# Performance work log

Measured on AMD Instinct MI355X. Metric: run time of the kernel, lower is better.

Reference implementation:

```python
import jax, jax.numpy as jnp
import numpy as np

NUM_GRAPHS = 64
BN_EPS = 1e-5
N, E, F_IN, ED, HID, HEADS, NC = 50000, 1600000, 128, 16, 32, 2, 2


def gatv2(x, src, dst, edge_attr, Wl, bl, Wr, br, We, att, bias, num_nodes):
    """PyG GATv2Conv: gather, leaky-relu score, segment softmax over dst, scatter-sum."""
    H, C = att.shape
    xl = (x @ Wl + bl).reshape(num_nodes, H, C)  # source transform (lin_l)
    xr = (x @ Wr + br).reshape(num_nodes, H, C)  # target transform (lin_r)
    ef = (edge_attr @ We).reshape(-1, H, C)      # [E,H,C]
    m = xl[src] + xr[dst] + ef                   # per-edge message pre-activation
    m = jnp.where(m > 0, m, 0.2 * m)             # LeakyReLU(0.2)
    score = jnp.einsum('ehc,hc->eh', m, att)     # [E,H]
    smax = jax.ops.segment_max(score, dst, num_segments=num_nodes)
    smax = jnp.where(jnp.isfinite(smax), smax, 0.0)
    ex = jnp.exp(score - smax[dst])
    denom = jax.ops.segment_sum(ex, dst, num_segments=num_nodes)
    alpha = ex / (denom[dst] + 1e-16)            # segment softmax
    out = jax.ops.segment_sum(xl[src] * alpha[..., None], dst, num_segments=num_nodes)
    return out.reshape(num_nodes, H * C) + bias


def batchnorm(x, gamma, beta, mean, var):
    # inference-mode BatchNorm1d with running statistics
    return (x - mean) * gamma * jax.lax.rsqrt(var + BN_EPS) + beta


def setup_inputs() -> dict:
    keys = jax.random.split(jax.random.key(0), 40)
    ki = iter(keys)

    def glorot(shape):
        return jax.random.normal(next(ki), shape, jnp.float32) / np.sqrt(shape[0])

    def bn_params(dim):
        g = jax.random.uniform(next(ki), (dim,), jnp.float32, 0.5, 1.5)
        b = jax.random.normal(next(ki), (dim,), jnp.float32) * 0.1
        m = jax.random.normal(next(ki), (dim,), jnp.float32) * 0.1
        v = jax.random.uniform(next(ki), (dim,), jnp.float32, 0.5, 1.5)
        return g, b, m, v

    x = jax.random.normal(next(ki), (N, F_IN), jnp.float32)
    edge_index = jax.random.randint(next(ki), (2, E), 0, N)
    edge_attr = jax.random.normal(next(ki), (E, ED), jnp.float32)
    batch = jnp.sort(jax.random.randint(next(ki), (N,), 0, NUM_GRAPHS))

    d1 = HID * HEADS  # 64
    inp = dict(x=x, edge_attr=edge_attr, edge_index=edge_index, batch=batch)
    # conv1: in=F_IN, heads=HEADS, out=HID
    inp.update(c1_Wl=glorot((F_IN, d1)), c1_bl=jnp.zeros((d1,), jnp.float32),
               c1_Wr=glorot((F_IN, d1)), c1_br=jnp.zeros((d1,), jnp.float32),
               c1_We=glorot((ED, d1)),
               c1_att=jax.random.normal(next(ki), (HEADS, HID), jnp.float32) / np.sqrt(HID),
               c1_bias=jnp.zeros((d1,), jnp.float32))
    g, b, m, v = bn_params(d1)
    inp.update(bn1_gamma=g, bn1_beta=b, bn1_mean=m, bn1_var=v)
    inp.update(sp1_W=glorot((F_IN, d1)), sp1_b=jnp.zeros((d1,), jnp.float32))
    # conv2: in=d1, heads=1, out=HID
    inp.update(c2_Wl=glorot((d1, HID)), c2_bl=jnp.zeros((HID,), jnp.float32),
               c2_Wr=glorot((d1, HID)), c2_br=jnp.zeros((HID,), jnp.float32),
               c2_We=glorot((ED, HID)),
               c2_att=jax.random.normal(next(ki), (1, HID), jnp.float32) / np.sqrt(HID),
               c2_bias=jnp.zeros((HID,), jnp.float32))
    g, b, m, v = bn_params(HID)
    inp.update(bn2_gamma=g, bn2_beta=b, bn2_mean=m, bn2_var=v)
    inp.update(sp2_W=glorot((d1, HID)), sp2_b=jnp.zeros((HID,), jnp.float32))
    inp.update(cls_W=glorot((2 * HID, NC)), cls_b=jnp.zeros((NC,), jnp.float32))
    return inp


def reference(x, edge_attr,
              c1_Wl, c1_bl, c1_Wr, c1_br, c1_We, c1_att, c1_bias,
              bn1_gamma, bn1_beta, bn1_mean, bn1_var, sp1_W, sp1_b,
              c2_Wl, c2_bl, c2_Wr, c2_br, c2_We, c2_att, c2_bias,
              bn2_gamma, bn2_beta, bn2_mean, bn2_var, sp2_W, sp2_b,
              cls_W, cls_b, edge_index, batch):
    num_nodes = x.shape[0]
    src, dst = edge_index[0], edge_index[1]

    xp = x @ sp1_W + sp1_b
    h = gatv2(x, src, dst, edge_attr, c1_Wl, c1_bl, c1_Wr, c1_br, c1_We, c1_att, c1_bias, num_nodes)
    h = batchnorm(h, bn1_gamma, bn1_beta, bn1_mean, bn1_var)
    h = jax.nn.elu(h + xp)

    xp = h @ sp2_W + sp2_b
    h2 = gatv2(h, src, dst, edge_attr, c2_Wl, c2_bl, c2_Wr, c2_br, c2_We, c2_att, c2_bias, num_nodes)
    h2 = batchnorm(h2, bn2_gamma, bn2_beta, bn2_mean, bn2_var)
    h2 = jax.nn.elu(h2 + xp)

    # global mean + max pool per graph
    cnt = jax.ops.segment_sum(jnp.ones((num_nodes, 1), h2.dtype), batch, num_segments=NUM_GRAPHS)
    gmean = jax.ops.segment_sum(h2, batch, num_segments=NUM_GRAPHS) / jnp.maximum(cnt, 1.0)
    gmax = jax.ops.segment_max(h2, batch, num_segments=NUM_GRAPHS)
    gmax = jnp.where(jnp.isfinite(gmax), gmax, 0.0)
    g = jnp.concatenate([gmean, gmax], axis=1)
    # dropout is identity in eval mode
    return g @ cls_W + cls_b
```

## Files before the change

### kernel.cpp

```cpp
#include <hip/hip_runtime.h>
#include <math.h>

#define NN 50000
#define NE 1600000
#define FIN 128
#define EDIM 16
#define DD1 64
#define HH1 2
#define DD2 32
#define NG 64
#define NCLS 2
#define SCAN_CHUNK 512
#define NB_SCAN ((NN + SCAN_CHUNK - 1) / SCAN_CHUNK)

template<int IN, int OUT>
__global__ __launch_bounds__(256) void transform_k(const float* __restrict__ X,
    const float* __restrict__ W, const float* __restrict__ b,
    float* __restrict__ out, int n) {
  constexpr int NPB = 32;
  constexpr int TPN = 256 / NPB;
  constexpr int CPT = OUT / TPN;
  __shared__ float sW[IN * OUT];
  __shared__ float sX[NPB * IN];
  int t = threadIdx.x;
  int nodeBase = blockIdx.x * NPB;
  for (int i = t; i < IN * OUT; i += 256) sW[i] = W[i];
  constexpr int XE = NPB * IN / 4;
  const float4* X4 = (const float4*)X;
  float4* sX4 = (float4*)sX;
  for (int i = t; i < XE; i += 256) {
    int node = nodeBase + i / (IN / 4);
    sX4[i] = (node < n) ? X4[(size_t)node * (IN / 4) + i % (IN / 4)]
                        : make_float4(0.f, 0.f, 0.f, 0.f);
  }
  __syncthreads();
  int ln = t / TPN;
  int cb = (t % TPN) * CPT;
  int node = nodeBase + ln;
  float acc[CPT];
#pragma unroll
  for (int j = 0; j < CPT; j++) acc[j] = b[cb + j];
  const float* xs = &sX[ln * IN];
  for (int k = 0; k < IN; k++) {
    float xv = xs[k];
#pragma unroll
    for (int j = 0; j < CPT; j++) acc[j] += xv * sW[k * OUT + cb + j];
  }
  if (node < n) {
#pragma unroll
    for (int j = 0; j < CPT; j++) out[(size_t)node * OUT + cb + j] = acc[j];
  }
}

__global__ __launch_bounds__(256) void hist_k(const int* __restrict__ ei, int* __restrict__ deg) {
  int e = blockIdx.x * 256 + threadIdx.x;
  if (e >= NE) return;
  atomicAdd(&deg[ei[NE + e]], 1);
}

__global__ __launch_bounds__(256) void scan_bsum_k(const int* __restrict__ deg,
                                                   int* __restrict__ bsum, int n) {
  __shared__ int s[256];
  int b = blockIdx.x, t = threadIdx.x;
  int i0 = b * SCAN_CHUNK + 2 * t, i1 = i0 + 1;
  int v = ((i0 < n) ? deg[i0] : 0) + ((i1 < n) ? deg[i1] : 0);
  s[t] = v;
  __syncthreads();
  for (int off = 128; off; off >>= 1) {
    if (t < off) s[t] += s[t + off];
    __syncthreads();
  }
  if (t == 0) bsum[b] = s[0];
}

__global__ void scan_boff_k(const int* __restrict__ bsum, int* __restrict__ boff, int nb) {
  if (threadIdx.x == 0) {
    int run = 0;
    for (int i = 0; i < nb; i++) { int v = bsum[i]; boff[i] = run; run += v; }
  }
}

__global__ __launch_bounds__(256) void scan_rowptr_k(const int* __restrict__ deg,
    const int* __restrict__ boff, int* __restrict__ rowptr, int n) {
  __shared__ int s[256];
  int b = blockIdx.x, t = threadIdx.x;
  int i0 = b * SCAN_CHUNK + 2 * t, i1 = i0 + 1;
  int d0 = (i0 < n) ? deg[i0] : 0;
  int d1 = (i1 < n) ? deg[i1] : 0;
  s[t] = d0 + d1;
  __syncthreads();
  for (int off = 1; off < 256; off <<= 1) {
    int add = (t >= off) ? s[t - off] : 0;
    __syncthreads();
    s[t] += add;
    __syncthreads();
  }
  int excl = (t == 0) ? 0 : s[t - 1];
  int o = boff[b] + excl;
  if (i0 < n) rowptr[i0] = o;
  if (i1 < n) rowptr[i1] = o + d0;
}

__global__ __launch_bounds__(256) void fill_k(const int* __restrict__ ei,
    const int* __restrict__ rowptr, int* __restrict__ fillc,
    int* __restrict__ srcs_perm, int* __restrict__ posmap) {
  int e = blockIdx.x * 256 + threadIdx.x;
  if (e >= NE) return;
  int src = ei[e], dst = ei[NE + e];
  int pos = rowptr[dst] + atomicAdd(&fillc[dst], 1);
  srcs_perm[pos] = src;
  posmap[e] = pos;
}

template<int D, int H>
__global__ __launch_bounds__(256) void score_k(
    const int* __restrict__ ei, const float* __restrict__ eattr,
    const float* __restrict__ xl, const float* __restrict__ xr,
    const float* __restrict__ We, const float* __restrict__ att,
    const int* __restrict__ posmap, float* __restrict__ ex_perm) {
  constexpr int C = D / H;
  __shared__ float sWe[EDIM * D];
  __shared__ float sAtt[D];
  int t = threadIdx.x;
  for (int i = t; i < EDIM * D; i += 256) sWe[i] = We[i];
  for (int i = t; i < D; i += 256) sAtt[i] = att[i];
  __syncthreads();
  int e = blockIdx.x * 256 + t;
  if (e >= NE) return;
  int src = ei[e], dst = ei[NE + e];
  float ea[EDIM];
  const float4* ea4 = (const float4*)(eattr + (size_t)e * EDIM);
#pragma unroll
  for (int q = 0; q < EDIM / 4; q++) {
    float4 v = ea4[q];
    ea[4 * q] = v.x; ea[4 * q + 1] = v.y; ea[4 * q + 2] = v.z; ea[4 * q + 3] = v.w;
  }
  const float4* xls = (const float4*)(xl + (size_t)src * D);
  const float4* xrd = (const float4*)(xr + (size_t)dst * D);
  float sc[H];
#pragma unroll
  for (int h = 0; h < H; h++) sc[h] = 0.f;
#pragma unroll
  for (int q = 0; q < D / 4; q++) {
    float4 a = xls[q], r = xrd[q];
    float av[4] = {a.x, a.y, a.z, a.w};
    float rv[4] = {r.x, r.y, r.z, r.w};
#pragma unroll
    for (int j = 0; j < 4; j++) {
      int hc = 4 * q + j;
      float ef = 0.f;
#pragma unroll
      for (int k = 0; k < EDIM; k++) ef += ea[k] * sWe[k * D + hc];
      float m = av[j] + rv[j] + ef;
      m = m > 0.f ? m : 0.2f * m;
      sc[hc / C] += m * sAtt[hc];
    }
  }
  int pos = posmap[e];
#pragma unroll
  for (int h = 0; h < H; h++) ex_perm[(size_t)pos * H + h] = expf(sc[h]);
}

template<int D, int H>
__global__ __launch_bounds__(256) void gather_k(
    const int* __restrict__ rowptr, const int* __restrict__ deg,
    const int* __restrict__ srcs_perm, const float* __restrict__ ex_perm,
    const float* __restrict__ xl, const float* __restrict__ bias,
    const float* __restrict__ gamma, const float* __restrict__ beta,
    const float* __restrict__ mean, const float* __restrict__ var,
    const float* __restrict__ xp, float* __restrict__ hout) {
  constexpr int C = D / H;
  int gid = (blockIdx.x * 256 + threadIdx.x) / D;
  int lane = threadIdx.x % D;
  if (gid >= NN) return;
  int start = rowptr[gid];
  int len = deg[gid];
  float den[H];
#pragma unroll
  for (int h = 0; h < H; h++) den[h] = 0.f;
  for (int j = lane; j < len; j += D) {
#pragma unroll
    for (int h = 0; h < H; h++) den[h] += ex_perm[(size_t)(start + j) * H + h];
  }
#pragma unroll
  for (int off = D / 2; off; off >>= 1) {
#pragma unroll
    for (int h = 0; h < H; h++) den[h] += __shfl_xor(den[h], off, D);
  }
  float inv[H];
#pragma unroll
  for (int h = 0; h < H; h++) inv[h] = 1.f / (den[h] + 1e-16f);
  int h = lane / C;
  float myinv = inv[h];
  float acc = 0.f;
  for (int j = 0; j < len; j++) {
    int src = srcs_perm[start + j];
    float exv = ex_perm[(size_t)(start + j) * H + h];
    acc += xl[(size_t)src * D + lane] * (exv * myinv);
  }
  float v = acc + bias[lane];
  v = (v - mean[lane]) * gamma[lane] * rsqrtf(var[lane] + 1e-5f) + beta[lane];
  v += xp[(size_t)gid * D + lane];
  hout[(size_t)gid * D + lane] = v > 0.f ? v : expm1f(v);
}

__device__ inline unsigned fkey(float f) {
  unsigned u = __float_as_uint(f);
  return (u & 0x80000000u) ? ~u : (u | 0x80000000u);
}
__device__ inline float funkey(unsigned k) {
  unsigned u = (k & 0x80000000u) ? (k & 0x7FFFFFFFu) : ~k;
  return __uint_as_float(u);
}

__global__ __launch_bounds__(256) void pool_init_k(float* sums, unsigned* maxk, int* cnt) {
  int t = blockIdx.x * 256 + threadIdx.x;
  if (t < NG * DD2) { sums[t] = 0.f; maxk[t] = fkey(-INFINITY); }
  if (t < NG) cnt[t] = 0;
}

#define PSPAN 16
__global__ __launch_bounds__(256) void pool_accum_k(const float* __restrict__ h2,
    const int* __restrict__ batch, float* sums, unsigned* maxk, int* cnt) {
  __shared__ float ls[PSPAN][DD2];
  __shared__ unsigned lm[PSPAN][DD2];
  __shared__ int lc[PSPAN];
  int base = blockIdx.x * 256;
  int t = threadIdx.x;
  int c = t % DD2;
  int nsub = t / DD2;
  int lastNode = min(base + 256, NN) - 1;
  int gmin = batch[base];
  int gmax = batch[lastNode];
  for (int gbase = gmin; gbase <= gmax; gbase += PSPAN) {
    int span = min(PSPAN, gmax - gbase + 1);
    for (int i = t; i < span * DD2; i += 256) {
      ls[i / DD2][i % DD2] = 0.f;
      lm[i / DD2][i % DD2] = fkey(-INFINITY);
    }
    if (t < span) lc[t] = 0;
    __syncthreads();
    for (int nnode = base + nsub; nnode < base + 256 && nnode < NN; nnode += 8) {
      int g = batch[nnode] - gbase;
      if (g >= 0 && g < span) {
        float v = h2[(size_t)nnode * DD2 + c];
        atomicAdd(&ls[g][c], v);
        atomicMax(&lm[g][c], fkey(v));
        if (c == 0) atomicAdd(&lc[g], 1);
      }
    }
    __syncthreads();
    for (int i = t; i < span * DD2; i += 256) {
      int g = gbase + i / DD2;
      atomicAdd(&sums[g * DD2 + i % DD2], ls[i / DD2][i % DD2]);
      atomicMax(&maxk[g * DD2 + i % DD2], lm[i / DD2][i % DD2]);
    }
    if (t < span) atomicAdd(&cnt[gbase + t], lc[t]);
    __syncthreads();
  }
}

__global__ void classify_k(const float* __restrict__ sums, const unsigned* __restrict__ maxk,
    const int* __restrict__ cnt, const float* __restrict__ W,
    const float* __restrict__ b, float* __restrict__ out) {
  int t = threadIdx.x;
  if (t >= NG * NCLS) return;
  int g = t / NCLS, k = t % NCLS;
  float accv = b[k];
  float inv = 1.f / fmaxf((float)cnt[g], 1.f);
  for (int j = 0; j < DD2; j++) accv += (sums[g * DD2 + j] * inv) * W[j * NCLS + k];
  for (int j = 0; j < DD2; j++) {
    float mx = funkey(maxk[g * DD2 + j]);
    if (mx < -3e38f) mx = 0.f;
    accv += mx * W[(DD2 + j) * NCLS + k];
  }
  out[g * NCLS + k] = accv;
}

extern "C" void kernel_launch(void* const* d_in, const int* in_sizes, int n_in,
                              void* d_out, int out_size, void* d_ws, size_t ws_size,
                              hipStream_t stream) {
  (void)in_sizes; (void)n_in; (void)out_size; (void)ws_size;
  const float* x       = (const float*)d_in[0];
  const float* eattr   = (const float*)d_in[1];
  const int*   ei      = (const int*)d_in[2];
  const int*   batch   = (const int*)d_in[3];
  const float* c1_Wl   = (const float*)d_in[4];
  const float* c1_bl   = (const float*)d_in[5];
  const float* c1_Wr   = (const float*)d_in[6];
  const float* c1_br   = (const float*)d_in[7];
  const float* c1_We   = (const float*)d_in[8];
  const float* c1_att  = (const float*)d_in[9];
  const float* c1_bias = (const float*)d_in[10];
  const float* bn1_g   = (const float*)d_in[11];
  const float* bn1_b   = (const float*)d_in[12];
  const float* bn1_m   = (const float*)d_in[13];
  const float* bn1_v   = (const float*)d_in[14];
  const float* sp1_W   = (const float*)d_in[15];
  const float* sp1_b   = (const float*)d_in[16];
  const float* c2_Wl   = (const float*)d_in[17];
  const float* c2_bl   = (const float*)d_in[18];
  const float* c2_Wr   = (const float*)d_in[19];
  const float* c2_br   = (const float*)d_in[20];
  const float* c2_We   = (const float*)d_in[21];
  const float* c2_att  = (const float*)d_in[22];
  const float* c2_bias = (const float*)d_in[23];
  const float* bn2_g   = (const float*)d_in[24];
  const float* bn2_b   = (const float*)d_in[25];
  const float* bn2_m   = (const float*)d_in[26];
  const float* bn2_v   = (const float*)d_in[27];
  const float* sp2_W   = (const float*)d_in[28];
  const float* sp2_b   = (const float*)d_in[29];
  const float* cls_W   = (const float*)d_in[30];
  const float* cls_b   = (const float*)d_in[31];

  float* w     = (float*)d_ws;
  float* A     = w;
  float* B     = A + (size_t)NN * DD1;
  float* Cb    = B + (size_t)NN * DD1;
  float* H1    = Cb + (size_t)NN * DD1;
  float* EXP   = H1 + (size_t)NN * DD1;
  int* srcs    = (int*)(EXP + (size_t)NE * HH1);
  int* posm    = srcs + NE;
  int* rowptr  = posm + NE;
  int* deg     = rowptr + NN;
  int* fillc   = deg + NN;
  int* bsum    = fillc + NN;
  int* boff    = bsum + NB_SCAN;
  float* PS    = (float*)(boff + NB_SCAN);
  unsigned* PM = (unsigned*)(PS + NG * DD2);
  int* PC      = (int*)(PM + NG * DD2);

  int tgrid = (NN + 31) / 32;
  int egrid = (NE + 255) / 256;

  hipMemsetAsync(deg, 0, (size_t)NN * sizeof(int), stream);
  hipMemsetAsync(fillc, 0, (size_t)NN * sizeof(int), stream);
  hist_k<<<egrid, 256, 0, stream>>>(ei, deg);
  scan_bsum_k<<<NB_SCAN, 256, 0, stream>>>(deg, bsum, NN);
  scan_boff_k<<<1, 64, 0, stream>>>(bsum, boff, NB_SCAN);
  scan_rowptr_k<<<NB_SCAN, 256, 0, stream>>>(deg, boff, rowptr, NN);
  fill_k<<<egrid, 256, 0, stream>>>(ei, rowptr, fillc, srcs, posm);

  transform_k<FIN, DD1><<<tgrid, 256, 0, stream>>>(x, c1_Wl, c1_bl, A, NN);
  transform_k<FIN, DD1><<<tgrid, 256, 0, stream>>>(x, c1_Wr, c1_br, B, NN);
  transform_k<FIN, DD1><<<tgrid, 256, 0, stream>>>(x, sp1_W, sp1_b, Cb, NN);
  score_k<DD1, HH1><<<egrid, 256, 0, stream>>>(ei, eattr, A, B, c1_We, c1_att, posm, EXP);
  gather_k<DD1, HH1><<<(NN * DD1 + 255) / 256, 256, 0, stream>>>(
      rowptr, deg, srcs, EXP, A, c1_bias, bn1_g, bn1_b, bn1_m, bn1_v, Cb, H1);

  transform_k<DD1, DD2><<<tgrid, 256, 0, stream>>>(H1, c2_Wl, c2_bl, A, NN);
  transform_k<DD1, DD2><<<tgrid, 256, 0, stream>>>(H1, c2_Wr, c2_br, B, NN);
  transform_k<DD1, DD2><<<tgrid, 256, 0, stream>>>(H1, sp2_W, sp2_b, Cb, NN);
  score_k<DD2, 1><<<egrid, 256, 0, stream>>>(ei, eattr, A, B, c2_We, c2_att, posm, EXP);
  gather_k<DD2, 1><<<(NN * DD2 + 255) / 256, 256, 0, stream>>>(
      rowptr, deg, srcs, EXP, A, c2_bias, bn2_g, bn2_b, bn2_m, bn2_v, Cb, H1);

  pool_init_k<<<(NG * DD2 + 255) / 256, 256, 0, stream>>>(PS, PM, PC);
  pool_accum_k<<<(NN + 255) / 256, 256, 0, stream>>>(H1, batch, PS, PM, PC);
  classify_k<<<1, 128, 0, stream>>>(PS, PM, PC, cls_W, cls_b, (float*)d_out);
}
```

Measured before the change: 1.154 ms.

## Iterate score kernel in CSR order so writes and dst reads coalesce

The score kernel now walks edges in destination-sorted (CSR) order, using new dstv and eperm arrays written by fill_k, instead of the original edge order. The exp-score writes become contiguous, and because consecutive threads share the same dst, the xr reads hit cache. The cost is that edge_attr is now read through a random permutation, and fill_k writes two extra arrays. For H=2 the two scores are stored with a single float2 write.

```diff
diff --git a/kernel.cpp b/kernel.cpp
--- a/kernel.cpp
+++ b/kernel.cpp
@@ -103,21 +103,23 @@
 
 __global__ __launch_bounds__(256) void fill_k(const int* __restrict__ ei,
     const int* __restrict__ rowptr, int* __restrict__ fillc,
-    int* __restrict__ srcs_perm, int* __restrict__ posmap) {
+    int* __restrict__ srcs_perm, int* __restrict__ dstv, int* __restrict__ eperm) {
   int e = blockIdx.x * 256 + threadIdx.x;
   if (e >= NE) return;
   int src = ei[e], dst = ei[NE + e];
   int pos = rowptr[dst] + atomicAdd(&fillc[dst], 1);
   srcs_perm[pos] = src;
-  posmap[e] = pos;
+  dstv[pos] = dst;
+  eperm[pos] = e;
 }
 
 template<int D, int H>
-__global__ __launch_bounds__(256) void score_k(
-    const int* __restrict__ ei, const float* __restrict__ eattr,
+__global__ __launch_bounds__(256) void score_csr_k(
+    const int* __restrict__ srcs_perm, const int* __restrict__ dstv,
+    const int* __restrict__ eperm, const float* __restrict__ eattr,
     const float* __restrict__ xl, const float* __restrict__ xr,
     const float* __restrict__ We, const float* __restrict__ att,
-    const int* __restrict__ posmap, float* __restrict__ ex_perm) {
+    float* __restrict__ ex_perm) {
   constexpr int C = D / H;
   __shared__ float sWe[EDIM * D];
   __shared__ float sAtt[D];
@@ -125,9 +127,9 @@
   for (int i = t; i < EDIM * D; i += 256) sWe[i] = We[i];
   for (int i = t; i < D; i += 256) sAtt[i] = att[i];
   __syncthreads();
-  int e = blockIdx.x * 256 + t;
-  if (e >= NE) return;
-  int src = ei[e], dst = ei[NE + e];
+  int p = blockIdx.x * 256 + t;
+  if (p >= NE) return;
+  int src = srcs_perm[p], dst = dstv[p], e = eperm[p];
   float ea[EDIM];
   const float4* ea4 = (const float4*)(eattr + (size_t)e * EDIM);
 #pragma unroll
@@ -156,9 +158,13 @@
       sc[hc / C] += m * sAtt[hc];
     }
   }
-  int pos = posmap[e];
-#pragma unroll
-  for (int h = 0; h < H; h++) ex_perm[(size_t)pos * H + h] = expf(sc[h]);
+  if (H == 2) {
+    float2 ex2 = make_float2(expf(sc[0]), expf(sc[H - 1]));
+    *(float2*)&ex_perm[(size_t)p * 2] = ex2;
+  } else {
+#pragma unroll
+    for (int h = 0; h < H; h++) ex_perm[(size_t)p * H + h] = expf(sc[h]);
+  }
 }
 
 template<int D, int H>
@@ -321,8 +327,9 @@
   float* H1    = Cb + (size_t)NN * DD1;
   float* EXP   = H1 + (size_t)NN * DD1;
   int* srcs    = (int*)(EXP + (size_t)NE * HH1);
-  int* posm    = srcs + NE;
-  int* rowptr  = posm + NE;
+  int* dstv    = srcs + NE;
+  int* eperm   = dstv + NE;
+  int* rowptr  = eperm + NE;
   int* deg     = rowptr + NN;
   int* fillc   = deg + NN;
   int* bsum    = fillc + NN;
@@ -340,19 +347,19 @@
   scan_bsum_k<<<NB_SCAN, 256, 0, stream>>>(deg, bsum, NN);
   scan_boff_k<<<1, 64, 0, stream>>>(bsum, boff, NB_SCAN);
   scan_rowptr_k<<<NB_SCAN, 256, 0, stream>>>(deg, boff, rowptr, NN);
-  fill_k<<<egrid, 256, 0, stream>>>(ei, rowptr, fillc, srcs, posm);
+  fill_k<<<egrid, 256, 0, stream>>>(ei, rowptr, fillc, srcs, dstv, eperm);
 
   transform_k<FIN, DD1><<<tgrid, 256, 0, stream>>>(x, c1_Wl, c1_bl, A, NN);
   transform_k<FIN, DD1><<<tgrid, 256, 0, stream>>>(x, c1_Wr, c1_br, B, NN);
   transform_k<FIN, DD1><<<tgrid, 256, 0, stream>>>(x, sp1_W, sp1_b, Cb, NN);
-  score_k<DD1, HH1><<<egrid, 256, 0, stream>>>(ei, eattr, A, B, c1_We, c1_att, posm, EXP);
+  score_csr_k<DD1, HH1><<<egrid, 256, 0, stream>>>(srcs, dstv, eperm, eattr, A, B, c1_We, c1_att, EXP);
   gather_k<DD1, HH1><<<(NN * DD1 + 255) / 256, 256, 0, stream>>>(
       rowptr, deg, srcs, EXP, A, c1_bias, bn1_g, bn1_b, bn1_m, bn1_v, Cb, H1);
 
   transform_k<DD1, DD2><<<tgrid, 256, 0, stream>>>(H1, c2_Wl, c2_bl, A, NN);
   transform_k<DD1, DD2><<<tgrid, 256, 0, stream>>>(H1, c2_Wr, c2_br, B, NN);
   transform_k<DD1, DD2><<<tgrid, 256, 0, stream>>>(H1, sp2_W, sp2_b, Cb, NN);
-  score_k<DD2, 1><<<egrid, 256, 0, stream>>>(ei, eattr, A, B, c2_We, c2_att, posm, EXP);
+  score_csr_k<DD2, 1><<<egrid, 256, 0, stream>>>(srcs, dstv, eperm, eattr, A, B, c2_We, c2_att, EXP);
   gather_k<DD2, 1><<<(NN * DD2 + 255) / 256, 256, 0, stream>>>(
       rowptr, deg, srcs, EXP, A, c2_bias, bn2_g, bn2_b, bn2_m, bn2_v, Cb, H1);
 
```

Measured after the change: 1.028 ms. 10.9% less time.
